# Performance work log

Measured on AMD Instinct MI355X. Metric: run time of the kernel, lower is better.

The kernel has to match this reference:

```python
import jax, jax.numpy as jnp
import numpy as np

B, S, H = 2, 2048, 2304
NH, NKV, HD = 8, 4, 256
FF = 9216
SOFTCAP = 50.0
SCALE = 256.0 ** -0.5  # query_pre_attn_scalar ** -0.5
EPS = 1e-6
THETA = 10000.0


def setup_inputs() -> dict:
    key = jax.random.key(0)
    ks = jax.random.split(key, 13)
    s = 0.02
    x = jax.random.normal(ks[0], (B, S, H), jnp.float32)
    causal = jnp.tril(jnp.ones((S, S), bool))
    mask = jnp.where(causal, 0.0, -1e9).astype(jnp.float32)[None, None]  # [1,1,S,S]
    return {
        "x": x,
        "mask": mask,
        "wq": jax.random.normal(ks[1], (H, NH * HD), jnp.float32) * s,
        "wk": jax.random.normal(ks[2], (H, NKV * HD), jnp.float32) * s,
        "wv": jax.random.normal(ks[3], (H, NKV * HD), jnp.float32) * s,
        "wo": jax.random.normal(ks[4], (NH * HD, H), jnp.float32) * s,
        "w_gate": jax.random.normal(ks[5], (H, FF), jnp.float32) * s,
        "w_up": jax.random.normal(ks[6], (H, FF), jnp.float32) * s,
        "w_down": jax.random.normal(ks[7], (FF, H), jnp.float32) * s,
        "g_in": jax.random.normal(ks[8], (H,), jnp.float32) * 0.1,
        "g_post_attn": jax.random.normal(ks[9], (H,), jnp.float32) * 0.1,
        "g_pre_ff": jax.random.normal(ks[10], (H,), jnp.float32) * 0.1,
        "g_post_ff": jax.random.normal(ks[11], (H,), jnp.float32) * 0.1,
    }


def rmsnorm(x, g):
    # Gemma2RMSNorm: fp32 norm, (1 + weight) gain
    x32 = x.astype(jnp.float32)
    var = jnp.mean(x32 * x32, axis=-1, keepdims=True)
    return (x32 * jax.lax.rsqrt(var + EPS) * (1.0 + g.astype(jnp.float32))).astype(x.dtype)


def apply_rope(q, k):
    # q: [B,S,NH,HD], k: [B,S,NKV,HD]; positions 0..S-1 (start_pos=0)
    inv_freq = 1.0 / (THETA ** (jnp.arange(0, HD, 2, dtype=jnp.float32) / HD))
    t = jnp.arange(S, dtype=jnp.float32)
    freqs = jnp.outer(t, inv_freq)                 # [S, HD/2]
    emb = jnp.concatenate([freqs, freqs], axis=-1)  # [S, HD]
    cos = jnp.cos(emb)[None, :, None, :]
    sin = jnp.sin(emb)[None, :, None, :]

    def rot_half(v):
        return jnp.concatenate([-v[..., HD // 2:], v[..., : HD // 2]], axis=-1)

    return q * cos + rot_half(q) * sin, k * cos + rot_half(k) * sin


def reference(x, mask, wq, wk, wv, wo, w_gate, w_up, w_down,
              g_in, g_post_attn, g_pre_ff, g_post_ff):
    # --- attention sub-block ---
    h = rmsnorm(x, g_in)
    q = (h @ wq).reshape(B, S, NH, HD)
    k = (h @ wk).reshape(B, S, NKV, HD)
    v = (h @ wv).reshape(B, S, NKV, HD)
    q, k = apply_rope(q, k)
    rep = NH // NKV
    k = jnp.repeat(k, rep, axis=2)  # [B,S,NH,HD]
    v = jnp.repeat(v, rep, axis=2)
    scores = jnp.einsum('bqhd,bkhd->bhqk', q, k) * SCALE
    scores = SOFTCAP * jnp.tanh(scores / SOFTCAP)  # logit soft-capping
    scores = scores + mask
    p = jax.nn.softmax(scores, axis=-1)
    o = jnp.einsum('bhqk,bkhd->bqhd', p, v).reshape(B, S, NH * HD)
    attn_out = o @ wo
    h2 = x + rmsnorm(attn_out, g_post_attn)
    # --- GeGLU MLP sub-block ---
    f = rmsnorm(h2, g_pre_ff)
    mlp = (jax.nn.gelu(f @ w_gate, approximate=True) * (f @ w_up)) @ w_down
    return h2 + rmsnorm(mlp, g_post_ff)
```

## Files before the change

kernel.cpp:

```cpp
#include <hip/hip_runtime.h>
#include <hip/hip_bf16.h>
#include <cstdint>
#include <cstddef>

typedef __bf16 bf16;
typedef __bf16 bf16x8 __attribute__((ext_vector_type(8)));
typedef __bf16 bf16x4v __attribute__((ext_vector_type(4)));
typedef float f32x4 __attribute__((ext_vector_type(4)));

#define NB 2
#define NS 2048
#define NHID 2304
#define NHEADS 8
#define NKVH 4
#define HDIM 256
#define NFF 9216
#define NROWS (NB * NS)
#define SCALE_F 0.0625f
#define SOFTCAP_F 50.0f

#define ASYNC16(ldsp, gp)                                                     \
    __builtin_amdgcn_global_load_lds(                                         \
        (__attribute__((address_space(1))) void*)(gp),                        \
        (__attribute__((address_space(3))) void*)(ldsp), 16, 0, 0)

__device__ __forceinline__ float fast_tanh(float x) {
    x = fminf(fmaxf(x, -10.f), 10.f);
    float e = __expf(2.f * x);
    return (e - 1.f) / (e + 1.f);
}

__global__ __launch_bounds__(256)
void transpose_cvt_part(const float* __restrict__ W, int N, int k0,
                        bf16* __restrict__ dst, int dstK, int dstOff) {
    __shared__ float tile[64][65];
    const int ntiles = N >> 6;
    const int tk = blockIdx.x / ntiles, tn = blockIdx.x % ntiles;
    const int kk0 = k0 + (tk << 6), n0 = tn << 6;
    const int tr = threadIdx.x >> 4, tc = threadIdx.x & 15;
#pragma unroll
    for (int j = 0; j < 4; ++j) {
        const int r = j * 16 + tr;
        const float4 v = *(const float4*)&W[(size_t)(kk0 + r) * N + n0 + tc * 4];
        tile[r][tc * 4 + 0] = v.x; tile[r][tc * 4 + 1] = v.y;
        tile[r][tc * 4 + 2] = v.z; tile[r][tc * 4 + 3] = v.w;
    }
    __syncthreads();
#pragma unroll
    for (int j = 0; j < 4; ++j) {
        const int n = j * 16 + tr;
        bf16x4v o;
        o.x = (bf16)tile[tc * 4 + 0][n];
        o.y = (bf16)tile[tc * 4 + 1][n];
        o.z = (bf16)tile[tc * 4 + 2][n];
        o.w = (bf16)tile[tc * 4 + 3][n];
        *(bf16x4v*)&dst[(size_t)(n0 + n) * dstK + dstOff + (tk << 6) + tc * 4] = o;
    }
}

__global__ __launch_bounds__(256)
void copy_expand(const bf16* __restrict__ src, bf16* __restrict__ dst,
                 int srcK, int dstK, int total) {
    const int idx = blockIdx.x * 256 + threadIdx.x;
    if (idx >= total) return;
    const int cpr = srcK >> 3;
    const int n = idx / cpr, c = idx % cpr;
    *(uint4*)&dst[(size_t)n * dstK + c * 8] = *(const uint4*)&src[(size_t)n * srcK + c * 8];
}

template <bool ADD, bool OBF>
__global__ __launch_bounds__(256)
void rmsnorm_k(const float* __restrict__ src, const float* __restrict__ res,
               const float* __restrict__ g, void* __restrict__ out) {
    const int row = blockIdx.x;
    const float* xr = src + (size_t)row * NHID;
    float vals[9];
    float ss = 0.f;
#pragma unroll
    for (int j = 0; j < 9; ++j) {
        vals[j] = xr[threadIdx.x + j * 256];
        ss += vals[j] * vals[j];
    }
#pragma unroll
    for (int off = 32; off > 0; off >>= 1) ss += __shfl_xor(ss, off);
    __shared__ float wss[4];
    if ((threadIdx.x & 63) == 0) wss[threadIdx.x >> 6] = ss;
    __syncthreads();
    const float scale = rsqrtf((wss[0] + wss[1] + wss[2] + wss[3]) * (1.f / NHID) + 1e-6f);
#pragma unroll
    for (int j = 0; j < 9; ++j) {
        const int c = threadIdx.x + j * 256;
        float v = vals[j] * scale * (1.f + g[c]);
        if constexpr (ADD) v += res[(size_t)row * NHID + c];
        if constexpr (OBF) ((bf16*)out)[(size_t)row * NHID + c] = (bf16)v;
        else               ((float*)out)[(size_t)row * NHID + c] = v;
    }
}

__global__ __launch_bounds__(256)
void rope_k(bf16* __restrict__ q, bf16* __restrict__ k) {
    const int idx = blockIdx.x * 256 + threadIdx.x;
    const int i = idx & 127;
    const int t = idx >> 7;
    const int head = t % 12;
    const int row = t / 12;
    const int s = row & (NS - 1);
    const float ang = (float)s * exp2f(-(float)i * 0.10381025296523007f);
    float sn, cs;
    sincosf(ang, &sn, &cs);
    bf16* base = (head < 8) ? (q + (size_t)row * 2048 + head * 256 + i)
                            : (k + (size_t)row * 1024 + (head - 8) * 256 + i);
    const float x1 = (float)base[0], x2 = (float)base[128];
    base[0]   = (bf16)(x1 * cs - x2 * sn);
    base[128] = (bf16)(x2 * cs + x1 * sn);
}

template <int MODE>
__global__ __launch_bounds__(256)
void gemm_bt(const bf16* __restrict__ A, const bf16* __restrict__ Bt,
             void* __restrict__ C, int M, int N, int K) {
    __shared__ __align__(16) bf16 As[128 * 32];
    __shared__ __align__(16) bf16 Bs[128 * 32];
    const int tid = threadIdx.x;
    const int lane = tid & 63, wave = tid >> 6;
    const int lq = lane & 15, quad = lane >> 4;
    const int ntiles = N >> 7;
    const int tm = blockIdx.x / ntiles, tn = blockIdx.x % ntiles;
    const int m0 = tm << 7, n0 = tn << 7;
    const int wrow = (wave >> 1) << 6, wcol = (wave & 1) << 6;
    f32x4 acc[4][4];
#pragma unroll
    for (int i = 0; i < 4; ++i)
#pragma unroll
        for (int j = 0; j < 4; ++j) acc[i][j] = (f32x4){0.f, 0.f, 0.f, 0.f};

    const int wr0 = wave * 32;
    const int lrow = lane >> 2, lcol = (lane & 3) * 8;

    for (int k0 = 0; k0 < K; k0 += 32) {
        __syncthreads();
        const bf16* ga = &A[(size_t)(m0 + wr0 + lrow) * K + k0 + lcol];
        const bf16* gb = &Bt[(size_t)(n0 + wr0 + lrow) * K + k0 + lcol];
#pragma unroll
        for (int j = 0; j < 2; ++j) {
            ASYNC16(&As[(wr0 + j * 16) * 32], ga + (size_t)(j * 16) * K);
            ASYNC16(&Bs[(wr0 + j * 16) * 32], gb + (size_t)(j * 16) * K);
        }
        __syncthreads();
        bf16x8 af[4], bfr[4];
#pragma unroll
        for (int i = 0; i < 4; ++i) {
            af[i]  = *(const bf16x8*)&As[(wrow + i * 16 + lq) * 32 + quad * 8];
            bfr[i] = *(const bf16x8*)&Bs[(wcol + i * 16 + lq) * 32 + quad * 8];
        }
#pragma unroll
        for (int mi = 0; mi < 4; ++mi)
#pragma unroll
            for (int ni = 0; ni < 4; ++ni)
                acc[mi][ni] = __builtin_amdgcn_mfma_f32_16x16x32_bf16(af[mi], bfr[ni], acc[mi][ni], 0, 0, 0);
    }
#pragma unroll
    for (int mi = 0; mi < 4; ++mi) {
        const int r0 = m0 + wrow + mi * 16 + quad * 4;
#pragma unroll
        for (int ni = 0; ni < 4; ++ni) {
            const int cc = n0 + wcol + ni * 16 + lq;
#pragma unroll
            for (int i = 0; i < 4; ++i) {
                const float v = acc[mi][ni][i];
                if constexpr (MODE == 0) {
                    ((float*)C)[(size_t)(r0 + i) * N + cc] = v;
                } else if constexpr (MODE == 1) {
                    ((bf16*)C)[(size_t)(r0 + i) * N + cc] = (bf16)v;
                } else {
                    const int m = r0 + i, bb = m >> 11, ss = m & 2047;
                    ((bf16*)C)[((size_t)bb * N + cc) * 2048 + ss] = (bf16)v;
                }
            }
        }
    }
}

__device__ __forceinline__ int ldsoff(int row, int s) {
    return (row << 6) + (((s ^ row) & 7) << 3);
}

__device__ __forceinline__ void stage_tile(const bf16* __restrict__ Ag,
                                           const bf16* __restrict__ Bg,
                                           bf16* as, bf16* bs,
                                           int K, int k0, int w, int l) {
    const int rsub = l >> 3;
    const int koff = k0 + (((l & 7) ^ rsub) << 3);
    const int r0 = w * 8 + rsub;
#pragma unroll
    for (int c = 0; c < 4; ++c)
        ASYNC16(as + (c * 64 + w * 8) * 64, &Ag[(size_t)(c * 64 + r0) * K + koff]);
#pragma unroll
    for (int c = 0; c < 2; ++c)
        ASYNC16(bs + (c * 64 + w * 8) * 64, &Bg[(size_t)(c * 64 + r0) * K + koff]);
}

template <int MODE>
__global__ __launch_bounds__(512, 2)
void gemm256(const bf16* __restrict__ A, const bf16* __restrict__ Bt,
             void* __restrict__ C, const bf16* __restrict__ gate,
             int M, int N, int K) {
    __shared__ __align__(16) bf16 lds[3 * 24576];
    const int tid = threadIdx.x;
    const int l = tid & 63, w = tid >> 6;
    const int lq = l & 15, quad = l >> 4;
    const int wm = w >> 1, wn = w & 1;

    const int ntm = M >> 8;
    const int nwg = gridDim.x, bid = blockIdx.x;
    const int q8 = nwg >> 3, r8 = nwg & 7;
    const int xcd = bid & 7, loc = bid >> 3;
    const int wg = (xcd < r8 ? xcd * (q8 + 1) : r8 * (q8 + 1) + (xcd - r8) * q8) + loc;
    const int tm = wg % ntm, tn = wg / ntm;

    const bf16* Ab = A  + (size_t)(tm << 8) * K;
    const bf16* Bb = Bt + (size_t)(tn << 7) * K;

    const int NT = K >> 6;
    stage_tile(Ab, Bb, lds, lds + 16384, K, 0, w, l);
    stage_tile(Ab, Bb, lds + 24576, lds + 24576 + 16384, K, 64, w, l);
    asm volatile("s_waitcnt vmcnt(6)" ::: "memory");
    __builtin_amdgcn_s_barrier();
    __builtin_amdgcn_sched_barrier(0);

    f32x4 acc[4][4];
#pragma unroll
    for (int i = 0; i < 4; ++i)
#pragma unroll
        for (int j = 0; j < 4; ++j) acc[i][j] = (f32x4){0.f, 0.f, 0.f, 0.f};

    int b = 0;
    for (int t = 0; t < NT; ++t) {
        bf16* as = lds + b * 24576;
        bf16* bs = as + 16384;
        if (t + 2 < NT) {
            int b2 = b + 2; if (b2 >= 3) b2 -= 3;
            stage_tile(Ab, Bb, lds + b2 * 24576, lds + b2 * 24576 + 16384,
                       K, (t + 2) << 6, w, l);
        }
#pragma unroll
        for (int kk = 0; kk < 2; ++kk) {
            bf16x8 af[4], bfr[4];
#pragma unroll
            for (int i = 0; i < 4; ++i)
                af[i]  = *(const bf16x8*)&as[ldsoff(wm * 64 + i * 16 + lq, kk * 4 + quad)];
#pragma unroll
            for (int i = 0; i < 4; ++i)
                bfr[i] = *(const bf16x8*)&bs[ldsoff(wn * 64 + i * 16 + lq, kk * 4 + quad)];
            __builtin_amdgcn_s_setprio(1);
#pragma unroll
            for (int mi = 0; mi < 4; ++mi)
#pragma unroll
                for (int ni = 0; ni < 4; ++ni)
                    acc[mi][ni] = __builtin_amdgcn_mfma_f32_16x16x32_bf16(
                        af[mi], bfr[ni], acc[mi][ni], 0, 0, 0);
            __builtin_amdgcn_s_setprio(0);
        }
        if (t + 1 < NT) {
            if (t + 2 < NT) { asm volatile("s_waitcnt vmcnt(6)" ::: "memory"); }
            else            { asm volatile("s_waitcnt vmcnt(0)" ::: "memory"); }
            __builtin_amdgcn_s_barrier();
            __builtin_amdgcn_sched_barrier(0);
        }
        if (++b == 3) b = 0;
    }

    const int r0base = (tm << 8) + wm * 64 + quad * 4;
    const int c0base = (tn << 7) + wn * 64 + lq;
#pragma unroll
    for (int mi = 0; mi < 4; ++mi) {
#pragma unroll
        for (int ni = 0; ni < 4; ++ni) {
            const int cc = c0base + ni * 16;
#pragma unroll
            for (int i = 0; i < 4; ++i) {
                const int rr = r0base + mi * 16 + i;
                const size_t idx = (size_t)rr * N + cc;
                const float v = acc[mi][ni][i];
                if constexpr (MODE == 0) {
                    ((float*)C)[idx] = v;
                } else if constexpr (MODE == 1) {
                    ((bf16*)C)[idx] = (bf16)v;
                } else if constexpr (MODE == 3) {
                    const float inner = 0.7978845608028654f * (v + 0.044715f * v * v * v);
                    ((bf16*)C)[idx] = (bf16)(0.5f * v * (1.f + fast_tanh(inner)));
                } else {
                    ((bf16*)C)[idx] = (bf16)((float)gate[idx] * v);
                }
            }
        }
    }
}

__global__ __launch_bounds__(256)
void attn_k(const bf16* __restrict__ Q, const bf16* __restrict__ Kb,
            const bf16* __restrict__ Vt, bf16* __restrict__ O) {
    const int qt = blockIdx.x & 31;
    const int bh = blockIdx.x >> 5;
    const int h = bh & 7, b = bh >> 3;
    const int kvh = h >> 1;
    const int tid = threadIdx.x, lane = tid & 63, wave = tid >> 6;
    const int lq = lane & 15, quad = lane >> 4;

    __shared__ __align__(16) bf16 Ks[32 * 264];
    __shared__ __align__(16) bf16 VTs[256 * 40];
    __shared__ __align__(16) bf16 Ps[64 * 40];

    const bf16* qbase = Q + ((size_t)(b * NS + qt * 64)) * 2048 + h * 256;
    const bf16* kbase = Kb + (size_t)(b * NS) * 1024 + kvh * 256;
    const bf16* vbase = Vt + (size_t)b * 1024 * 2048 + (size_t)(kvh * 256) * 2048;

    bf16x8 aq[8];
#pragma unroll
    for (int ks = 0; ks < 8; ++ks)
        aq[ks] = *(const bf16x8*)&qbase[(size_t)(wave * 16 + lq) * 2048 + ks * 32 + quad * 8];

    f32x4 acco[16];
#pragma unroll
    for (int i = 0; i < 16; ++i) acco[i] = (f32x4){0.f, 0.f, 0.f, 0.f};
    float m_old[4] = {-1e30f, -1e30f, -1e30f, -1e30f};
    float l_old[4] = {0.f, 0.f, 0.f, 0.f};

    const int ktmax = 2 * qt + 1;
    for (int kt = 0; kt <= ktmax; ++kt) {
        __syncthreads();
#pragma unroll
        for (int j = 0; j < 4; ++j) {
            const int c = j * 256 + tid;
            const int r = c >> 5, c8 = (c & 31) * 8;
            *(uint4*)&Ks[r * 264 + c8] = *(const uint4*)&kbase[(size_t)(kt * 32 + r) * 1024 + c8];
        }
#pragma unroll
        for (int j = 0; j < 4; ++j) {
            const int c = j * 256 + tid;
            const int d = c >> 2, s8 = (c & 3) * 8;
            *(uint4*)&VTs[d * 40 + s8] = *(const uint4*)&vbase[(size_t)d * 2048 + kt * 32 + s8];
        }
        __syncthreads();

        f32x4 accs[2];
        accs[0] = (f32x4){0.f, 0.f, 0.f, 0.f};
        accs[1] = (f32x4){0.f, 0.f, 0.f, 0.f};
#pragma unroll
        for (int ks = 0; ks < 8; ++ks) {
#pragma unroll
            for (int nt = 0; nt < 2; ++nt) {
                const bf16x8 bk = *(const bf16x8*)&Ks[(nt * 16 + lq) * 264 + ks * 32 + quad * 8];
                accs[nt] = __builtin_amdgcn_mfma_f32_16x16x32_bf16(aq[ks], bk, accs[nt], 0, 0, 0);
            }
        }

        const bool diag = (kt >= 2 * qt);
        float p[2][4], rmax[4], rsum[4];
#pragma unroll
        for (int i = 0; i < 4; ++i) rmax[i] = -1e30f;
#pragma unroll
        for (int nt = 0; nt < 2; ++nt)
#pragma unroll
            for (int i = 0; i < 4; ++i) {
                float v = accs[nt][i] * SCALE_F;
                v = SOFTCAP_F * fast_tanh(v * (1.f / SOFTCAP_F));
                if (diag) {
                    const int qabs = qt * 64 + wave * 16 + quad * 4 + i;
                    const int kabs = kt * 32 + nt * 16 + lq;
                    if (kabs > qabs) v = -1e30f;
                }
                p[nt][i] = v;
                rmax[i] = fmaxf(rmax[i], v);
            }
#pragma unroll
        for (int i = 0; i < 4; ++i)
#pragma unroll
            for (int off = 8; off; off >>= 1) rmax[i] = fmaxf(rmax[i], __shfl_xor(rmax[i], off));

        float alpha[4];
#pragma unroll
        for (int i = 0; i < 4; ++i) {
            const float mn = fmaxf(m_old[i], rmax[i]);
            alpha[i] = __expf(m_old[i] - mn);
            m_old[i] = mn;
            rsum[i] = 0.f;
        }
#pragma unroll
        for (int nt = 0; nt < 2; ++nt)
#pragma unroll
            for (int i = 0; i < 4; ++i) {
                const float e = __expf(p[nt][i] - m_old[i]);
                p[nt][i] = e;
                rsum[i] += e;
            }
#pragma unroll
        for (int i = 0; i < 4; ++i) {
#pragma unroll
            for (int off = 8; off; off >>= 1) rsum[i] += __shfl_xor(rsum[i], off);
            l_old[i] = l_old[i] * alpha[i] + rsum[i];
        }
#pragma unroll
        for (int dt = 0; dt < 16; ++dt)
#pragma unroll
            for (int i = 0; i < 4; ++i) acco[dt][i] *= alpha[i];

#pragma unroll
        for (int nt = 0; nt < 2; ++nt)
#pragma unroll
            for (int i = 0; i < 4; ++i)
                Ps[(wave * 16 + quad * 4 + i) * 40 + nt * 16 + lq] = (bf16)p[nt][i];

        const bf16x8 ap = *(const bf16x8*)&Ps[(wave * 16 + lq) * 40 + quad * 8];
#pragma unroll
        for (int dt = 0; dt < 16; ++dt) {
            const bf16x8 bv = *(const bf16x8*)&VTs[(dt * 16 + lq) * 40 + quad * 8];
            acco[dt] = __builtin_amdgcn_mfma_f32_16x16x32_bf16(ap, bv, acco[dt], 0, 0, 0);
        }
    }

    bf16* obase = O + ((size_t)(b * NS + qt * 64 + wave * 16)) * 2048 + h * 256;
    float linv[4];
#pragma unroll
    for (int i = 0; i < 4; ++i) linv[i] = 1.f / l_old[i];
#pragma unroll
    for (int dt = 0; dt < 16; ++dt)
#pragma unroll
        for (int i = 0; i < 4; ++i)
            obase[(size_t)(quad * 4 + i) * 2048 + dt * 16 + lq] = (bf16)(acco[dt][i] * linv[i]);
}

extern "C" void kernel_launch(void* const* d_in, const int* in_sizes, int n_in,
                              void* d_out, int out_size, void* d_ws, size_t ws_size,
                              hipStream_t stream) {
    const float* x    = (const float*)d_in[0];
    float* wq   = (float*)d_in[2];
    float* wk   = (float*)d_in[3];
    float* wv   = (float*)d_in[4];
    float* wo   = (float*)d_in[5];
    float* wg   = (float*)d_in[6];
    float* wu   = (float*)d_in[7];
    float* wd   = (float*)d_in[8];
    const float* g_in = (const float*)d_in[9];
    const float* g_pa = (const float*)d_in[10];
    const float* g_pf = (const float*)d_in[11];
    const float* g_po = (const float*)d_in[12];
    float* out = (float*)d_out;

    uint8_t* ws = (uint8_t*)d_ws;
    size_t off = 0;
    auto alloc = [&](size_t bytes) {
        void* p = ws + off;
        off += (bytes + 255) & ~(size_t)255;
        return p;
    };
    bf16* temp   = (bf16*)alloc((size_t)9216 * 1152 * 2);
    bf16* h_bf   = (bf16*)alloc((size_t)NROWS * 2304 * 2);
    uint8_t* R   = (uint8_t*)alloc((size_t)NROWS * 9216 * 2);
    float* tmp1  = (float*)alloc((size_t)NROWS * 2304 * 4);
    float* h2    = (float*)alloc((size_t)NROWS * 2304 * 4);
    (void)ws_size; (void)in_sizes; (void)n_in; (void)out_size;

    bf16* q_bf   = (bf16*)R;
    bf16* k_bf   = (bf16*)(R + (size_t)16777216);
    bf16* v_t    = (bf16*)(R + (size_t)16777216 + 8388608);
    bf16* o_bf   = (bf16*)(R + (size_t)16777216 + 2 * 8388608);
    bf16* mlp_in = (bf16*)R;

    auto convert_weight = [&](float* W, int K, int N) {
        const int hK = K >> 1;
        const int blks = (hK >> 6) * (N >> 6);
        transpose_cvt_part<<<blks, 256, 0, stream>>>(W, N, 0, temp, hK, 0);
        transpose_cvt_part<<<blks, 256, 0, stream>>>(W, N, hK, (bf16*)W, K, hK);
        const int total = N * (hK >> 3);
        copy_expand<<<(total + 255) / 256, 256, 0, stream>>>(temp, (bf16*)W, hK, K, total);
    };
    convert_weight(wq, 2304, 2048);
    convert_weight(wk, 2304, 1024);
    convert_weight(wv, 2304, 1024);
    convert_weight(wo, 2048, 2304);
    convert_weight(wg, 2304, 9216);
    convert_weight(wu, 2304, 9216);
    convert_weight(wd, 9216, 2304);
    const bf16* wq_t = (const bf16*)wq;
    const bf16* wk_t = (const bf16*)wk;
    const bf16* wv_t = (const bf16*)wv;
    const bf16* wo_t = (const bf16*)wo;
    const bf16* wg_t = (const bf16*)wg;
    const bf16* wu_t = (const bf16*)wu;
    const bf16* wd_t = (const bf16*)wd;

    rmsnorm_k<false, true><<<NROWS, 256, 0, stream>>>(x, nullptr, g_in, h_bf);

    gemm256<1><<<16 * 16, 512, 0, stream>>>(h_bf, wq_t, q_bf, nullptr, NROWS, 2048, 2304);
    gemm_bt<1><<<32 * 8, 256, 0, stream>>>(h_bf, wk_t, k_bf, NROWS, 1024, 2304);
    gemm_bt<2><<<32 * 8, 256, 0, stream>>>(h_bf, wv_t, v_t, NROWS, 1024, 2304);

    rope_k<<<(NROWS * 12 * 128) / 256, 256, 0, stream>>>(q_bf, k_bf);

    attn_k<<<NB * NHEADS * (NS / 64), 256, 0, stream>>>(q_bf, k_bf, v_t, o_bf);

    gemm_bt<0><<<32 * 18, 256, 0, stream>>>(o_bf, wo_t, tmp1, NROWS, 2304, 2048);

    rmsnorm_k<true, false><<<NROWS, 256, 0, stream>>>(tmp1, x, g_pa, h2);
    rmsnorm_k<false, true><<<NROWS, 256, 0, stream>>>(h2, nullptr, g_pf, h_bf);

    gemm256<3><<<16 * 72, 512, 0, stream>>>(h_bf, wg_t, mlp_in, nullptr, NROWS, 9216, 2304);
    gemm256<4><<<16 * 72, 512, 0, stream>>>(h_bf, wu_t, mlp_in, mlp_in, NROWS, 9216, 2304);

    gemm_bt<0><<<32 * 18, 256, 0, stream>>>(mlp_in, wd_t, tmp1, NROWS, 2304, 9216);

    rmsnorm_k<true, false><<<NROWS, 256, 0, stream>>>(tmp1, h2, g_po, (void*)out);
}
```

Before: 1.690 ms.

## Replace GEMMs with 256x256 eight-wave pipelined kernel and fuse QKV projection

Replaces both the simple 128x128 gemm_bt and the 256x128 gemm256 with a single 256x256-tile kernel using 8 waves, 2x4 wave layout, double-buffered LDS staged in half-K slices interleaved with MFMA groups. Q, K and V projections are fused into one launch that routes output tiles to the right buffer (with transposed V layout). The intent is more data reuse per tile, fewer launches and better overlap of global loads with MFMA; it costs more accumulator registers, extra barriers per iteration, and fewer workgroups (144 tiles for the N=2304 GEMMs), which may underfill the 256 CUs.

New measurement: 1.562 ms. 7.6% less time.

```diff
diff --git a/kernel.cpp b/kernel.cpp
--- a/kernel.cpp
+++ b/kernel.cpp
@@ -115,101 +115,28 @@
     base[128] = (bf16)(x2 * cs + x1 * sn);
 }
 
-template <int MODE>
-__global__ __launch_bounds__(256)
-void gemm_bt(const bf16* __restrict__ A, const bf16* __restrict__ Bt,
-             void* __restrict__ C, int M, int N, int K) {
-    __shared__ __align__(16) bf16 As[128 * 32];
-    __shared__ __align__(16) bf16 Bs[128 * 32];
-    const int tid = threadIdx.x;
-    const int lane = tid & 63, wave = tid >> 6;
-    const int lq = lane & 15, quad = lane >> 4;
-    const int ntiles = N >> 7;
-    const int tm = blockIdx.x / ntiles, tn = blockIdx.x % ntiles;
-    const int m0 = tm << 7, n0 = tn << 7;
-    const int wrow = (wave >> 1) << 6, wcol = (wave & 1) << 6;
-    f32x4 acc[4][4];
-#pragma unroll
-    for (int i = 0; i < 4; ++i)
-#pragma unroll
-        for (int j = 0; j < 4; ++j) acc[i][j] = (f32x4){0.f, 0.f, 0.f, 0.f};
-
-    const int wr0 = wave * 32;
-    const int lrow = lane >> 2, lcol = (lane & 3) * 8;
-
-    for (int k0 = 0; k0 < K; k0 += 32) {
-        __syncthreads();
-        const bf16* ga = &A[(size_t)(m0 + wr0 + lrow) * K + k0 + lcol];
-        const bf16* gb = &Bt[(size_t)(n0 + wr0 + lrow) * K + k0 + lcol];
-#pragma unroll
-        for (int j = 0; j < 2; ++j) {
-            ASYNC16(&As[(wr0 + j * 16) * 32], ga + (size_t)(j * 16) * K);
-            ASYNC16(&Bs[(wr0 + j * 16) * 32], gb + (size_t)(j * 16) * K);
-        }
-        __syncthreads();
-        bf16x8 af[4], bfr[4];
-#pragma unroll
-        for (int i = 0; i < 4; ++i) {
-            af[i]  = *(const bf16x8*)&As[(wrow + i * 16 + lq) * 32 + quad * 8];
-            bfr[i] = *(const bf16x8*)&Bs[(wcol + i * 16 + lq) * 32 + quad * 8];
-        }
-#pragma unroll
-        for (int mi = 0; mi < 4; ++mi)
-#pragma unroll
-            for (int ni = 0; ni < 4; ++ni)
-                acc[mi][ni] = __builtin_amdgcn_mfma_f32_16x16x32_bf16(af[mi], bfr[ni], acc[mi][ni], 0, 0, 0);
-    }
-#pragma unroll
-    for (int mi = 0; mi < 4; ++mi) {
-        const int r0 = m0 + wrow + mi * 16 + quad * 4;
-#pragma unroll
-        for (int ni = 0; ni < 4; ++ni) {
-            const int cc = n0 + wcol + ni * 16 + lq;
-#pragma unroll
-            for (int i = 0; i < 4; ++i) {
-                const float v = acc[mi][ni][i];
-                if constexpr (MODE == 0) {
-                    ((float*)C)[(size_t)(r0 + i) * N + cc] = v;
-                } else if constexpr (MODE == 1) {
-                    ((bf16*)C)[(size_t)(r0 + i) * N + cc] = (bf16)v;
-                } else {
-                    const int m = r0 + i, bb = m >> 11, ss = m & 2047;
-                    ((bf16*)C)[((size_t)bb * N + cc) * 2048 + ss] = (bf16)v;
-                }
-            }
-        }
-    }
-}
-
-__device__ __forceinline__ int ldsoff(int row, int s) {
-    return (row << 6) + (((s ^ row) & 7) << 3);
-}
-
-__device__ __forceinline__ void stage_tile(const bf16* __restrict__ Ag,
-                                           const bf16* __restrict__ Bg,
-                                           bf16* as, bf16* bs,
-                                           int K, int k0, int w, int l) {
-    const int rsub = l >> 3;
-    const int koff = k0 + (((l & 7) ^ rsub) << 3);
-    const int r0 = w * 8 + rsub;
-#pragma unroll
-    for (int c = 0; c < 4; ++c)
-        ASYNC16(as + (c * 64 + w * 8) * 64, &Ag[(size_t)(c * 64 + r0) * K + koff]);
-#pragma unroll
-    for (int c = 0; c < 2; ++c)
-        ASYNC16(bs + (c * 64 + w * 8) * 64, &Bg[(size_t)(c * 64 + r0) * K + koff]);
+__device__ __forceinline__ void stage_half(const bf16* __restrict__ src,
+                                           bf16* lds_half, int K, int kcol0,
+                                           int w, int l) {
+    const int r = w * 16 + (l >> 2);
+    const int c = kcol0 + (l & 3) * 8;
+#pragma unroll
+    for (int j = 0; j < 2; ++j)
+        ASYNC16(lds_half + (j * 512 + w * 64) * 8,
+                src + (size_t)(j * 128 + r) * K + c);
 }
 
 template <int MODE>
 __global__ __launch_bounds__(512, 2)
-void gemm256(const bf16* __restrict__ A, const bf16* __restrict__ Bt,
-             void* __restrict__ C, const bf16* __restrict__ gate,
-             int M, int N, int K) {
-    __shared__ __align__(16) bf16 lds[3 * 24576];
+void gemm8p(const bf16* __restrict__ A, const bf16* __restrict__ B0,
+            const bf16* __restrict__ B1, const bf16* __restrict__ B2,
+            void* __restrict__ C0, bf16* __restrict__ C1, bf16* __restrict__ C2,
+            const bf16* __restrict__ gate, int M, int N, int K) {
+    __shared__ __align__(16) bf16 lds[2 * 32768];
     const int tid = threadIdx.x;
     const int l = tid & 63, w = tid >> 6;
     const int lq = l & 15, quad = l >> 4;
-    const int wm = w >> 1, wn = w & 1;
+    const int wm = w >> 2, wn = w & 3;
 
     const int ntm = M >> 8;
     const int nwg = gridDim.x, bid = blockIdx.x;
@@ -218,79 +145,110 @@
     const int wg = (xcd < r8 ? xcd * (q8 + 1) : r8 * (q8 + 1) + (xcd - r8) * q8) + loc;
     const int tm = wg % ntm, tn = wg / ntm;
 
-    const bf16* Ab = A  + (size_t)(tm << 8) * K;
-    const bf16* Bb = Bt + (size_t)(tn << 7) * K;
+    const bf16* Ab = A + (size_t)(tm << 8) * K;
+    const bf16* Bb;
+    int vreg = 0, col0 = tn << 8;
+    if constexpr (MODE == 5) {
+        if (tn < 8)       { Bb = B0 + (size_t)(tn << 8) * K;        vreg = 0; col0 = tn << 8; }
+        else if (tn < 12) { Bb = B1 + (size_t)((tn - 8) << 8) * K;  vreg = 1; col0 = (tn - 8) << 8; }
+        else              { Bb = B2 + (size_t)((tn - 12) << 8) * K; vreg = 2; col0 = (tn - 12) << 8; }
+    } else {
+        Bb = B0 + (size_t)(tn << 8) * K;
+    }
+
+    auto ldsA = [&](int buf, int kk) { return lds + buf * 32768 + kk * 8192; };
+    auto ldsB = [&](int buf, int kk) { return lds + buf * 32768 + 16384 + kk * 8192; };
 
     const int NT = K >> 6;
-    stage_tile(Ab, Bb, lds, lds + 16384, K, 0, w, l);
-    stage_tile(Ab, Bb, lds + 24576, lds + 24576 + 16384, K, 64, w, l);
-    asm volatile("s_waitcnt vmcnt(6)" ::: "memory");
+    stage_half(Ab, ldsA(0, 0), K, 0,  w, l);
+    stage_half(Bb, ldsB(0, 0), K, 0,  w, l);
+    stage_half(Ab, ldsA(0, 1), K, 32, w, l);
+    stage_half(Bb, ldsB(0, 1), K, 32, w, l);
+    stage_half(Ab, ldsA(1, 0), K, 64, w, l);
+    stage_half(Bb, ldsB(1, 0), K, 64, w, l);
+    asm volatile("s_waitcnt vmcnt(4)" ::: "memory");
+    __builtin_amdgcn_sched_barrier(0);
     __builtin_amdgcn_s_barrier();
     __builtin_amdgcn_sched_barrier(0);
 
-    f32x4 acc[4][4];
-#pragma unroll
-    for (int i = 0; i < 4; ++i)
+    f32x4 acc[8][4];
+#pragma unroll
+    for (int i = 0; i < 8; ++i)
 #pragma unroll
         for (int j = 0; j < 4; ++j) acc[i][j] = (f32x4){0.f, 0.f, 0.f, 0.f};
 
-    int b = 0;
     for (int t = 0; t < NT; ++t) {
-        bf16* as = lds + b * 24576;
-        bf16* bs = as + 16384;
-        if (t + 2 < NT) {
-            int b2 = b + 2; if (b2 >= 3) b2 -= 3;
-            stage_tile(Ab, Bb, lds + b2 * 24576, lds + b2 * 24576 + 16384,
-                       K, (t + 2) << 6, w, l);
-        }
+        const int b = t & 1;
+        bf16x8 bfr[4];
 #pragma unroll
         for (int kk = 0; kk < 2; ++kk) {
-            bf16x8 af[4], bfr[4];
-#pragma unroll
-            for (int i = 0; i < 4; ++i)
-                af[i]  = *(const bf16x8*)&as[ldsoff(wm * 64 + i * 16 + lq, kk * 4 + quad)];
-#pragma unroll
-            for (int i = 0; i < 4; ++i)
-                bfr[i] = *(const bf16x8*)&bs[ldsoff(wn * 64 + i * 16 + lq, kk * 4 + quad)];
-            __builtin_amdgcn_s_setprio(1);
-#pragma unroll
-            for (int mi = 0; mi < 4; ++mi)
-#pragma unroll
-                for (int ni = 0; ni < 4; ++ni)
-                    acc[mi][ni] = __builtin_amdgcn_mfma_f32_16x16x32_bf16(
-                        af[mi], bfr[ni], acc[mi][ni], 0, 0, 0);
-            __builtin_amdgcn_s_setprio(0);
-        }
-        if (t + 1 < NT) {
-            if (t + 2 < NT) { asm volatile("s_waitcnt vmcnt(6)" ::: "memory"); }
-            else            { asm volatile("s_waitcnt vmcnt(0)" ::: "memory"); }
-            __builtin_amdgcn_s_barrier();
-            __builtin_amdgcn_sched_barrier(0);
-        }
-        if (++b == 3) b = 0;
-    }
-
-    const int r0base = (tm << 8) + wm * 64 + quad * 4;
-    const int c0base = (tn << 7) + wn * 64 + lq;
-#pragma unroll
-    for (int mi = 0; mi < 4; ++mi) {
+            const bf16* Ah = ldsA(b, kk);
+            const bf16* Bh = ldsB(b, kk);
+#pragma unroll
+            for (int mh = 0; mh < 2; ++mh) {
+                bf16x8 af[4];
+#pragma unroll
+                for (int i = 0; i < 4; ++i)
+                    af[i] = *(const bf16x8*)&Ah[(wm * 128 + mh * 64 + i * 16 + lq) * 32 + quad * 8];
+                if (mh == 0) {
+#pragma unroll
+                    for (int i = 0; i < 4; ++i)
+                        bfr[i] = *(const bf16x8*)&Bh[(wn * 64 + i * 16 + lq) * 32 + quad * 8];
+                }
+                if (kk == 0 && mh == 0 && t + 1 < NT)
+                    stage_half(Ab, ldsA(b ^ 1, 1), K, ((t + 1) << 6) + 32, w, l);
+                if (kk == 0 && mh == 1 && t + 1 < NT)
+                    stage_half(Bb, ldsB(b ^ 1, 1), K, ((t + 1) << 6) + 32, w, l);
+                if (kk == 1 && mh == 0 && t + 2 < NT)
+                    stage_half(Ab, ldsA(b, 0), K, (t + 2) << 6, w, l);
+                if (kk == 1 && mh == 1 && t + 2 < NT)
+                    stage_half(Bb, ldsB(b, 0), K, (t + 2) << 6, w, l);
+                __builtin_amdgcn_sched_barrier(0);
+                __builtin_amdgcn_s_barrier();
+                __builtin_amdgcn_s_setprio(1);
+#pragma unroll
+                for (int mi = 0; mi < 4; ++mi)
+#pragma unroll
+                    for (int ni = 0; ni < 4; ++ni)
+                        acc[mh * 4 + mi][ni] = __builtin_amdgcn_mfma_f32_16x16x32_bf16(
+                            af[mi], bfr[ni], acc[mh * 4 + mi][ni], 0, 0, 0);
+                __builtin_amdgcn_s_setprio(0);
+                if (kk == 1 && mh == 1) {
+                    if (t + 2 < NT)      asm volatile("s_waitcnt vmcnt(4)" ::: "memory");
+                    else if (t + 1 < NT) asm volatile("s_waitcnt vmcnt(0)" ::: "memory");
+                }
+                __builtin_amdgcn_sched_barrier(0);
+                __builtin_amdgcn_s_barrier();
+                __builtin_amdgcn_sched_barrier(0);
+            }
+        }
+    }
+
+    const int r0base = (tm << 8) + wm * 128 + quad * 4;
+    const int c0base = col0 + wn * 64 + lq;
+#pragma unroll
+    for (int mi = 0; mi < 8; ++mi) {
 #pragma unroll
         for (int ni = 0; ni < 4; ++ni) {
             const int cc = c0base + ni * 16;
 #pragma unroll
             for (int i = 0; i < 4; ++i) {
                 const int rr = r0base + mi * 16 + i;
-                const size_t idx = (size_t)rr * N + cc;
                 const float v = acc[mi][ni][i];
                 if constexpr (MODE == 0) {
-                    ((float*)C)[idx] = v;
+                    ((float*)C0)[(size_t)rr * N + cc] = v;
                 } else if constexpr (MODE == 1) {
-                    ((bf16*)C)[idx] = (bf16)v;
+                    ((bf16*)C0)[(size_t)rr * N + cc] = (bf16)v;
                 } else if constexpr (MODE == 3) {
                     const float inner = 0.7978845608028654f * (v + 0.044715f * v * v * v);
-                    ((bf16*)C)[idx] = (bf16)(0.5f * v * (1.f + fast_tanh(inner)));
+                    ((bf16*)C0)[(size_t)rr * N + cc] = (bf16)(0.5f * v * (1.f + fast_tanh(inner)));
+                } else if constexpr (MODE == 4) {
+                    const size_t idx = (size_t)rr * N + cc;
+                    ((bf16*)C0)[idx] = (bf16)((float)gate[idx] * v);
                 } else {
-                    ((bf16*)C)[idx] = (bf16)((float)gate[idx] * v);
+                    if (vreg == 0)      ((bf16*)C0)[(size_t)rr * 2048 + cc] = (bf16)v;
+                    else if (vreg == 1) C1[(size_t)rr * 1024 + cc] = (bf16)v;
+                    else                C2[((size_t)(rr >> 11) * 1024 + cc) * 2048 + (rr & 2047)] = (bf16)v;
                 }
             }
         }
@@ -492,23 +450,31 @@
 
     rmsnorm_k<false, true><<<NROWS, 256, 0, stream>>>(x, nullptr, g_in, h_bf);
 
-    gemm256<1><<<16 * 16, 512, 0, stream>>>(h_bf, wq_t, q_bf, nullptr, NROWS, 2048, 2304);
-    gemm_bt<1><<<32 * 8, 256, 0, stream>>>(h_bf, wk_t, k_bf, NROWS, 1024, 2304);
-    gemm_bt<2><<<32 * 8, 256, 0, stream>>>(h_bf, wv_t, v_t, NROWS, 1024, 2304);
+    gemm8p<5><<<16 * 16, 512, 0, stream>>>(h_bf, wq_t, wk_t, wv_t,
+                                           q_bf, k_bf, v_t, nullptr,
+                                           NROWS, 4096, 2304);
 
     rope_k<<<(NROWS * 12 * 128) / 256, 256, 0, stream>>>(q_bf, k_bf);
 
     attn_k<<<NB * NHEADS * (NS / 64), 256, 0, stream>>>(q_bf, k_bf, v_t, o_bf);
 
-    gemm_bt<0><<<32 * 18, 256, 0, stream>>>(o_bf, wo_t, tmp1, NROWS, 2304, 2048);
+    gemm8p<0><<<16 * 9, 512, 0, stream>>>(o_bf, wo_t, nullptr, nullptr,
+                                          tmp1, nullptr, nullptr, nullptr,
+                                          NROWS, 2304, 2048);
 
     rmsnorm_k<true, false><<<NROWS, 256, 0, stream>>>(tmp1, x, g_pa, h2);
     rmsnorm_k<false, true><<<NROWS, 256, 0, stream>>>(h2, nullptr, g_pf, h_bf);
 
-    gemm256<3><<<16 * 72, 512, 0, stream>>>(h_bf, wg_t, mlp_in, nullptr, NROWS, 9216, 2304);
-    gemm256<4><<<16 * 72, 512, 0, stream>>>(h_bf, wu_t, mlp_in, mlp_in, NROWS, 9216, 2304);
-
-    gemm_bt<0><<<32 * 18, 256, 0, stream>>>(mlp_in, wd_t, tmp1, NROWS, 2304, 9216);
+    gemm8p<3><<<16 * 36, 512, 0, stream>>>(h_bf, wg_t, nullptr, nullptr,
+                                           mlp_in, nullptr, nullptr, nullptr,
+                                           NROWS, 9216, 2304);
+    gemm8p<4><<<16 * 36, 512, 0, stream>>>(h_bf, wu_t, nullptr, nullptr,
+                                           mlp_in, nullptr, nullptr, mlp_in,
+                                           NROWS, 9216, 2304);
+
+    gemm8p<0><<<16 * 9, 512, 0, stream>>>(mlp_in, wd_t, nullptr, nullptr,
+                                          tmp1, nullptr, nullptr, nullptr,
+                                          NROWS, 2304, 9216);
 
     rmsnorm_k<true, false><<<NROWS, 256, 0, stream>>>(tmp1, h2, g_po, (void*)out);
 }
```
